# Performance work log

Measured on AMD Instinct MI355X. Metric: run time of the kernel, lower is better.

## Reference

```python
import jax, jax.numpy as jnp
import numpy as np

N_USERS = 100000
N_MOVIES = 100000
N_EDGES = 1000000
HIDDEN = 128


def setup_inputs() -> dict:
    key = jax.random.key(0)
    k1, k2, k3, k4, k5, k6, k7 = jax.random.split(key, 7)
    user_features = jax.random.normal(k1, (N_USERS, HIDDEN), dtype=jnp.float32)
    movie_features = jax.random.normal(k2, (N_MOVIES, HIDDEN), dtype=jnp.float32)
    src = jax.random.randint(k3, (N_EDGES,), 0, N_USERS, dtype=jnp.int64 if jax.config.jax_enable_x64 else jnp.int32)
    dst = jax.random.randint(k4, (N_EDGES,), 0, N_MOVIES, dtype=jnp.int64 if jax.config.jax_enable_x64 else jnp.int32)
    edge_index = jnp.stack([src, dst], axis=0)
    # Linear(2*HIDDEN, HIDDEN) params, torch-style init (kaiming uniform ~ U(-1/sqrt(fan_in), 1/sqrt(fan_in)))
    b1_bound = 1.0 / np.sqrt(2 * HIDDEN)
    W1 = jax.random.uniform(k5, (2 * HIDDEN, HIDDEN), minval=-b1_bound, maxval=b1_bound, dtype=jnp.float32)
    b1 = jax.random.uniform(k6, (HIDDEN,), minval=-b1_bound, maxval=b1_bound, dtype=jnp.float32)
    b2_bound = 1.0 / np.sqrt(HIDDEN)
    k8, k9 = jax.random.split(k7)
    W2 = jax.random.uniform(k8, (HIDDEN, 1), minval=-b2_bound, maxval=b2_bound, dtype=jnp.float32)
    b2 = jax.random.uniform(k9, (1,), minval=-b2_bound, maxval=b2_bound, dtype=jnp.float32)
    return {"user_features": user_features, "movie_features": movie_features,
            "edge_index": edge_index, "W1": W1, "b1": b1, "W2": W2, "b2": b2}


def reference(user_features, movie_features, edge_index, W1, b1, W2, b2):
    # Gather endpoint features per edge: [E, H] each
    u = user_features[edge_index[0]]
    m = movie_features[edge_index[1]]
    edge_feats = jnp.concatenate([u, m], axis=1)  # [E, 2H]
    h = jax.nn.relu(edge_feats @ W1 + b1)         # [E, H]
    out = h @ W2 + b2                             # [E, 1]
    return out.reshape(-1)
```

## Files before the change

### kernel.cpp

```cpp
#include <hip/hip_runtime.h>
#include <hip/hip_bf16.h>

typedef short s8v __attribute__((ext_vector_type(8)));
typedef float f4v __attribute__((ext_vector_type(4)));

__device__ __forceinline__ unsigned int bfround(float f) {
    unsigned int x = __float_as_uint(f);
    return (x + 0x7fffu + ((x >> 16) & 1u)) >> 16;
}

__device__ __forceinline__ float i8f(unsigned int w, int k) {
    return (float)((int)(signed char)(w >> (8 * k)));
}

__global__ __launch_bounds__(256) void pack_w(const float* __restrict__ W1,
                                              uint4* __restrict__ WF)
{
    const int half = blockIdx.x;
    #pragma unroll
    for (int iter = 0; iter < 8; ++iter) {
        int idx  = iter * 256 + threadIdx.x;
        int lane = idx & 63;
        int t    = (idx >> 6) & 7;
        int c    = idx >> 9;
        int q = lane >> 4, m = lane & 15;
        unsigned int w[4];
        #pragma unroll
        for (int jj = 0; jj < 4; ++jj) {
            float lo = W1[(size_t)(half * 128 + c * 32 + q * 8 + 2 * jj    ) * 128 + t * 16 + m];
            float hi = W1[(size_t)(half * 128 + c * 32 + q * 8 + 2 * jj + 1) * 128 + t * 16 + m];
            w[jj] = bfround(lo) | (bfround(hi) << 16);
        }
        WF[(size_t)half * 2048 + idx] = make_uint4(w[0], w[1], w[2], w[3]);
    }
}

__global__ __launch_bounds__(256, 3) void proj_kernel(
    const float* __restrict__ userf, const float* __restrict__ movief,
    const uint4* __restrict__ WF, const float* __restrict__ b1,
    uint2* __restrict__ Pu, uint2* __restrict__ Pm,
    float* __restrict__ SU, float* __restrict__ SM, int ntiles)
{
    const int half = blockIdx.x & 1;
    const int tile = (blockIdx.x >> 1) * 4 + (threadIdx.x >> 6);
    if (tile >= ntiles) return;
    const float* __restrict__ feat = half ? movief : userf;
    uint2* __restrict__ P = half ? Pm : Pu;
    float* __restrict__ S = half ? SM : SU;

    const int lane = threadIdx.x & 63;
    const int m    = lane & 15;
    const int q    = lane >> 4;

    const float4* arow = (const float4*)feat + (size_t)tile * 512;
    float4 a[4][2];
    #pragma unroll
    for (int c = 0; c < 4; ++c) {
        a[c][0] = arow[m * 32 + c * 8 + q * 2 + 0];
        a[c][1] = arow[m * 32 + c * 8 + q * 2 + 1];
    }

    float bias_v[8];
    #pragma unroll
    for (int t = 0; t < 8; ++t)
        bias_v[t] = half ? b1[t * 16 + m] : 0.0f;

    f4v acc[8];
    #pragma unroll
    for (int t = 0; t < 8; ++t)
        acc[t] = (f4v){bias_v[t], bias_v[t], bias_v[t], bias_v[t]};

    const uint4* wf = WF + (size_t)half * 2048;
    #pragma unroll
    for (int c = 0; c < 4; ++c) {
        uint4 fr[8];
        #pragma unroll
        for (int t = 0; t < 8; ++t)
            fr[t] = wf[(c * 8 + t) * 64 + lane];

        s8v af;
        af[0] = (short)bfround(a[c][0].x); af[1] = (short)bfround(a[c][0].y);
        af[2] = (short)bfround(a[c][0].z); af[3] = (short)bfround(a[c][0].w);
        af[4] = (short)bfround(a[c][1].x); af[5] = (short)bfround(a[c][1].y);
        af[6] = (short)bfround(a[c][1].z); af[7] = (short)bfround(a[c][1].w);

        #pragma unroll
        for (int t = 0; t < 8; ++t)
            acc[t] = __builtin_amdgcn_mfma_f32_16x16x32_bf16(af, *(const s8v*)&fr[t], acc[t], 0, 0, 0);
    }

    #pragma unroll
    for (int r = 0; r < 4; ++r) {
        float mx = 0.0f;
        #pragma unroll
        for (int t = 0; t < 8; ++t) mx = fmaxf(mx, fabsf(acc[t][r]));
        #pragma unroll
        for (int off = 1; off < 16; off <<= 1)
            mx = fmaxf(mx, __shfl_xor(mx, off, 64));
        float inv = mx > 0.0f ? 127.0f / mx : 0.0f;

        unsigned int lo = 0, hi = 0;
        #pragma unroll
        for (int t = 0; t < 4; ++t) {
            lo |= ((unsigned int)(__float2int_rn(acc[t][r]     * inv) & 0xff)) << (8 * t);
            hi |= ((unsigned int)(__float2int_rn(acc[t + 4][r] * inv) & 0xff)) << (8 * t);
        }
        int row = tile * 16 + q * 4 + r;
        P[(size_t)row * 16 + m] = make_uint2(lo, hi);
        if (m == 0) S[row] = mx * (1.0f / 127.0f);
    }
}

__global__ __launch_bounds__(256) void edge_kernel(
    const int* __restrict__ src, const int* __restrict__ dst,
    const uint2* __restrict__ Pu, const uint2* __restrict__ Pm,
    const float* __restrict__ SU, const float* __restrict__ SM,
    const float* __restrict__ W2, const float* __restrict__ b2,
    float* __restrict__ out)
{
    const int lane = threadIdx.x & 63;
    const int L    = lane & 15;
    const int g    = lane >> 4;
    const int eg   = (blockIdx.x * 4 + (threadIdx.x >> 6)) * 16 + g * 4;

    float w2v[8];
    #pragma unroll
    for (int j = 0; j < 8; ++j) w2v[j] = W2[j * 16 + L];

    int si[4], di[4];
    #pragma unroll
    for (int i = 0; i < 4; ++i) { si[i] = src[eg + i]; di[i] = dst[eg + i]; }

    uint2 pu[4], pm[4];
    float scu[4], scm[4];
    #pragma unroll
    for (int i = 0; i < 4; ++i) {
        pu[i] = Pu[(size_t)si[i] * 16 + L];
        pm[i] = Pm[(size_t)di[i] * 16 + L];
        scu[i] = SU[si[i]];
        scm[i] = SM[di[i]];
    }

    float res[4];
    #pragma unroll
    for (int i = 0; i < 4; ++i) {
        const unsigned int uw[2] = {pu[i].x, pu[i].y};
        const unsigned int mw[2] = {pm[i].x, pm[i].y};
        float acc = 0.0f;
        #pragma unroll
        for (int v = 0; v < 2; ++v) {
            #pragma unroll
            for (int k = 0; k < 4; ++k) {
                float h = fmaf(scu[i], i8f(uw[v], k), scm[i] * i8f(mw[v], k));
                acc = fmaf(fmaxf(h, 0.0f), w2v[v * 4 + k], acc);
            }
        }
        #pragma unroll
        for (int off = 1; off < 16; off <<= 1)
            acc += __shfl_xor(acc, off, 64);
        res[i] = acc;
    }

    if (L == 0) {
        float bb = b2[0];
        *(float4*)(out + eg) = make_float4(res[0] + bb, res[1] + bb, res[2] + bb, res[3] + bb);
    }
}

extern "C" void kernel_launch(void* const* d_in, const int* in_sizes, int n_in,
                              void* d_out, int out_size, void* d_ws, size_t ws_size,
                              hipStream_t stream) {
    const float* userf  = (const float*)d_in[0];
    const float* movief = (const float*)d_in[1];
    const int*   eidx   = (const int*)d_in[2];
    const float* W1     = (const float*)d_in[3];
    const float* b1     = (const float*)d_in[4];
    const float* W2     = (const float*)d_in[5];
    const float* b2     = (const float*)d_in[6];
    float* out = (float*)d_out;

    const int NU = in_sizes[0] / 128;
    const int NM = in_sizes[1] / 128;
    const int E  = in_sizes[2] / 2;

    uint2* Pu = (uint2*)d_ws;
    uint2* Pm = Pu + (size_t)NU * 16;
    float* SU = (float*)(Pm + (size_t)NM * 16);
    float* SM = SU + NU;
    uint4* WF = (uint4*)(SM + NM);

    const int ntiles = NU / 16;
    const int nblk   = 2 * ((ntiles + 3) / 4);

    pack_w<<<2, 256, 0, stream>>>(W1, WF);
    proj_kernel<<<nblk, 256, 0, stream>>>(userf, movief, WF, b1, Pu, Pm, SU, SM, ntiles);
    edge_kernel<<<E / 64, 256, 0, stream>>>(eidx, eidx + E, Pu, Pm, SU, SM, W2, b2, out);
}
```

Baseline: 192.9 us.

## Make projection kernel persistent with prefetch of next tile's features

The projection kernel now launches a fixed 1024 blocks, and each wave loops over tiles in a grid-stride pattern. While it computes the current tile, it loads the feature rows for the next one, so global-load latency overlaps with MFMA work. The per-element bf16 rounding is also replaced by the packed __float22bfloat162_rn conversion. The launch-bounds occupancy hint is dropped, and the prefetch buffer adds register pressure that could lower occupancy.

Result: no change. 192.3 us (-0.3%).

```diff
diff --git a/kernel.cpp b/kernel.cpp
--- a/kernel.cpp
+++ b/kernel.cpp
@@ -8,7 +8,10 @@
     unsigned int x = __float_as_uint(f);
     return (x + 0x7fffu + ((x >> 16) & 1u)) >> 16;
 }
-
+__device__ __forceinline__ unsigned int pkbf(float x, float y) {
+    __hip_bfloat162 h = __float22bfloat162_rn(make_float2(x, y));
+    return *(unsigned int*)&h;
+}
 __device__ __forceinline__ float i8f(unsigned int w, int k) {
     return (float)((int)(signed char)(w >> (8 * k)));
 }
@@ -35,80 +38,103 @@
     }
 }
 
-__global__ __launch_bounds__(256, 3) void proj_kernel(
+__global__ __launch_bounds__(256) void proj_kernel(
     const float* __restrict__ userf, const float* __restrict__ movief,
     const uint4* __restrict__ WF, const float* __restrict__ b1,
     uint2* __restrict__ Pu, uint2* __restrict__ Pm,
-    float* __restrict__ SU, float* __restrict__ SM, int ntiles)
+    float* __restrict__ SU, float* __restrict__ SM,
+    int ntiles, int bph)
 {
-    const int half = blockIdx.x & 1;
-    const int tile = (blockIdx.x >> 1) * 4 + (threadIdx.x >> 6);
-    if (tile >= ntiles) return;
+    const int half = blockIdx.x >= bph;
+    const int bid  = half ? blockIdx.x - bph : blockIdx.x;
     const float* __restrict__ feat = half ? movief : userf;
     uint2* __restrict__ P = half ? Pm : Pu;
     float* __restrict__ S = half ? SM : SU;
+    const uint4* __restrict__ wf = WF + (size_t)half * 2048;
 
     const int lane = threadIdx.x & 63;
     const int m    = lane & 15;
     const int q    = lane >> 4;
 
-    const float4* arow = (const float4*)feat + (size_t)tile * 512;
-    float4 a[4][2];
-    #pragma unroll
-    for (int c = 0; c < 4; ++c) {
-        a[c][0] = arow[m * 32 + c * 8 + q * 2 + 0];
-        a[c][1] = arow[m * 32 + c * 8 + q * 2 + 1];
-    }
-
     float bias_v[8];
     #pragma unroll
     for (int t = 0; t < 8; ++t)
         bias_v[t] = half ? b1[t * 16 + m] : 0.0f;
 
-    f4v acc[8];
-    #pragma unroll
-    for (int t = 0; t < 8; ++t)
-        acc[t] = (f4v){bias_v[t], bias_v[t], bias_v[t], bias_v[t]};
-
-    const uint4* wf = WF + (size_t)half * 2048;
-    #pragma unroll
-    for (int c = 0; c < 4; ++c) {
-        uint4 fr[8];
+    const int wid = bid * 4 + (threadIdx.x >> 6);
+    const int nw  = bph * 4;
+
+#define LOAD_A(dst, t_) do {                                          \
+        const float4* arow_ = (const float4*)feat + (size_t)(t_) * 512; \
+        _Pragma("unroll")                                             \
+        for (int c_ = 0; c_ < 4; ++c_) {                              \
+            dst[c_][0] = arow_[m * 32 + c_ * 8 + q * 2 + 0];          \
+            dst[c_][1] = arow_[m * 32 + c_ * 8 + q * 2 + 1];          \
+        }                                                             \
+    } while (0)
+
+    float4 a[4][2];
+    int tile = wid;
+    if (tile < ntiles) LOAD_A(a, tile);
+
+    while (tile < ntiles) {
+        const int nxt = tile + nw;
+        float4 an[4][2];
+        if (nxt < ntiles) LOAD_A(an, nxt);
+
+        f4v acc[8];
         #pragma unroll
         for (int t = 0; t < 8; ++t)
-            fr[t] = wf[(c * 8 + t) * 64 + lane];
-
-        s8v af;
-        af[0] = (short)bfround(a[c][0].x); af[1] = (short)bfround(a[c][0].y);
-        af[2] = (short)bfround(a[c][0].z); af[3] = (short)bfround(a[c][0].w);
-        af[4] = (short)bfround(a[c][1].x); af[5] = (short)bfround(a[c][1].y);
-        af[6] = (short)bfround(a[c][1].z); af[7] = (short)bfround(a[c][1].w);
-
-        #pragma unroll
-        for (int t = 0; t < 8; ++t)
-            acc[t] = __builtin_amdgcn_mfma_f32_16x16x32_bf16(af, *(const s8v*)&fr[t], acc[t], 0, 0, 0);
-    }
-
-    #pragma unroll
-    for (int r = 0; r < 4; ++r) {
-        float mx = 0.0f;
-        #pragma unroll
-        for (int t = 0; t < 8; ++t) mx = fmaxf(mx, fabsf(acc[t][r]));
-        #pragma unroll
-        for (int off = 1; off < 16; off <<= 1)
-            mx = fmaxf(mx, __shfl_xor(mx, off, 64));
-        float inv = mx > 0.0f ? 127.0f / mx : 0.0f;
-
-        unsigned int lo = 0, hi = 0;
-        #pragma unroll
-        for (int t = 0; t < 4; ++t) {
-            lo |= ((unsigned int)(__float2int_rn(acc[t][r]     * inv) & 0xff)) << (8 * t);
-            hi |= ((unsigned int)(__float2int_rn(acc[t + 4][r] * inv) & 0xff)) << (8 * t);
-        }
-        int row = tile * 16 + q * 4 + r;
-        P[(size_t)row * 16 + m] = make_uint2(lo, hi);
-        if (m == 0) S[row] = mx * (1.0f / 127.0f);
-    }
+            acc[t] = (f4v){bias_v[t], bias_v[t], bias_v[t], bias_v[t]};
+
+        #pragma unroll
+        for (int c = 0; c < 4; ++c) {
+            uint4 fr[8];
+            #pragma unroll
+            for (int t = 0; t < 8; ++t)
+                fr[t] = wf[(c * 8 + t) * 64 + lane];
+
+            uint4 aw;
+            aw.x = pkbf(a[c][0].x, a[c][0].y);
+            aw.y = pkbf(a[c][0].z, a[c][0].w);
+            aw.z = pkbf(a[c][1].x, a[c][1].y);
+            aw.w = pkbf(a[c][1].z, a[c][1].w);
+            s8v af = *(const s8v*)&aw;
+
+            #pragma unroll
+            for (int t = 0; t < 8; ++t)
+                acc[t] = __builtin_amdgcn_mfma_f32_16x16x32_bf16(af, *(const s8v*)&fr[t], acc[t], 0, 0, 0);
+        }
+
+        #pragma unroll
+        for (int r = 0; r < 4; ++r) {
+            float mx = 0.0f;
+            #pragma unroll
+            for (int t = 0; t < 8; ++t) mx = fmaxf(mx, fabsf(acc[t][r]));
+            #pragma unroll
+            for (int off = 1; off < 16; off <<= 1)
+                mx = fmaxf(mx, __shfl_xor(mx, off, 64));
+            float inv = mx > 0.0f ? 127.0f / mx : 0.0f;
+
+            unsigned int lo = 0, hi = 0;
+            #pragma unroll
+            for (int t = 0; t < 4; ++t) {
+                lo |= ((unsigned int)(__float2int_rn(acc[t][r]     * inv) & 0xff)) << (8 * t);
+                hi |= ((unsigned int)(__float2int_rn(acc[t + 4][r] * inv) & 0xff)) << (8 * t);
+            }
+            int row = tile * 16 + q * 4 + r;
+            P[(size_t)row * 16 + m] = make_uint2(lo, hi);
+            if (m == 0) S[row] = mx * (1.0f / 127.0f);
+        }
+
+        #pragma unroll
+        for (int c = 0; c < 4; ++c) {
+            a[c][0] = an[c][0];
+            a[c][1] = an[c][1];
+        }
+        tile = nxt;
+    }
+#undef LOAD_A
 }
 
 __global__ __launch_bounds__(256) void edge_kernel(
@@ -190,9 +216,9 @@
     uint4* WF = (uint4*)(SM + NM);
 
     const int ntiles = NU / 16;
-    const int nblk   = 2 * ((ntiles + 3) / 4);
+    const int bph    = 512;
 
     pack_w<<<2, 256, 0, stream>>>(W1, WF);
-    proj_kernel<<<nblk, 256, 0, stream>>>(userf, movief, WF, b1, Pu, Pm, SU, SM, ntiles);
+    proj_kernel<<<2 * bph, 256, 0, stream>>>(userf, movief, WF, b1, Pu, Pm, SU, SM, ntiles, bph);
     edge_kernel<<<E / 64, 256, 0, stream>>>(eidx, eidx + E, Pu, Pm, SU, SM, W2, b2, out);
 }
```

## Stage feature tiles through LDS with coalesced loads and packed bf16 conversion

Applied to the files above, without the earlier changes.

The projection kernel now loads each 16-row feature tile with fully coalesced float4 reads, converts pairs to bf16 with the packed intrinsic, and stores them to a padded LDS buffer. Each wave then reads its MFMA A-fragment from LDS, replacing the earlier strided per-lane global reads. Block-to-half mapping changes from interleaved to contiguous ranges, and the occupancy hint in launch bounds is dropped. The cost is 18KB of LDS per block plus extra LDS traffic, and there is no barrier because each wave only touches its own slice.

Result: no change. 189.9 us (-1.5%).

```diff
diff --git a/kernel.cpp b/kernel.cpp
--- a/kernel.cpp
+++ b/kernel.cpp
@@ -8,7 +8,10 @@
     unsigned int x = __float_as_uint(f);
     return (x + 0x7fffu + ((x >> 16) & 1u)) >> 16;
 }
-
+__device__ __forceinline__ unsigned int pkbf(float x, float y) {
+    __hip_bfloat162 h = __float22bfloat162_rn(make_float2(x, y));
+    return *(unsigned int*)&h;
+}
 __device__ __forceinline__ float i8f(unsigned int w, int k) {
     return (float)((int)(signed char)(w >> (8 * k)));
 }
@@ -35,54 +38,56 @@
     }
 }
 
-__global__ __launch_bounds__(256, 3) void proj_kernel(
+__global__ __launch_bounds__(256) void proj_kernel(
     const float* __restrict__ userf, const float* __restrict__ movief,
     const uint4* __restrict__ WF, const float* __restrict__ b1,
     uint2* __restrict__ Pu, uint2* __restrict__ Pm,
-    float* __restrict__ SU, float* __restrict__ SM, int ntiles)
+    float* __restrict__ SU, float* __restrict__ SM,
+    int ntiles, int bph)
 {
-    const int half = blockIdx.x & 1;
-    const int tile = (blockIdx.x >> 1) * 4 + (threadIdx.x >> 6);
+    __shared__ __align__(16) unsigned int lds[4608];
+
+    const int w    = threadIdx.x >> 6;
+    const int lane = threadIdx.x & 63;
+    const int half = blockIdx.x >= bph;
+    const int bid  = half ? blockIdx.x - bph : blockIdx.x;
+    const int tile = bid * 4 + w;
     if (tile >= ntiles) return;
+
     const float* __restrict__ feat = half ? movief : userf;
     uint2* __restrict__ P = half ? Pm : Pu;
     float* __restrict__ S = half ? SM : SU;
-
-    const int lane = threadIdx.x & 63;
-    const int m    = lane & 15;
-    const int q    = lane >> 4;
-
-    const float4* arow = (const float4*)feat + (size_t)tile * 512;
-    float4 a[4][2];
-    #pragma unroll
-    for (int c = 0; c < 4; ++c) {
-        a[c][0] = arow[m * 32 + c * 8 + q * 2 + 0];
-        a[c][1] = arow[m * 32 + c * 8 + q * 2 + 1];
-    }
-
-    float bias_v[8];
-    #pragma unroll
-    for (int t = 0; t < 8; ++t)
-        bias_v[t] = half ? b1[t * 16 + m] : 0.0f;
+    const uint4* __restrict__ wfh = WF + (size_t)half * 2048;
+
+    unsigned int* wl = lds + w * 1152;
+
+    const float4* tbase = (const float4*)feat + (size_t)tile * 512;
+    #pragma unroll
+    for (int p = 0; p < 8; ++p) {
+        float4 v = tbase[p * 64 + lane];
+        int r  = (p * 64 + lane) >> 5;
+        int cc = lane & 31;
+        *(uint2*)&wl[r * 72 + cc * 2] = make_uint2(pkbf(v.x, v.y), pkbf(v.z, v.w));
+    }
+
+    const int m = lane & 15;
+    const int q = lane >> 4;
 
     f4v acc[8];
     #pragma unroll
-    for (int t = 0; t < 8; ++t)
-        acc[t] = (f4v){bias_v[t], bias_v[t], bias_v[t], bias_v[t]};
-
-    const uint4* wf = WF + (size_t)half * 2048;
+    for (int t = 0; t < 8; ++t) {
+        float bv = half ? b1[t * 16 + m] : 0.0f;
+        acc[t] = (f4v){bv, bv, bv, bv};
+    }
+
     #pragma unroll
     for (int c = 0; c < 4; ++c) {
         uint4 fr[8];
         #pragma unroll
         for (int t = 0; t < 8; ++t)
-            fr[t] = wf[(c * 8 + t) * 64 + lane];
-
-        s8v af;
-        af[0] = (short)bfround(a[c][0].x); af[1] = (short)bfround(a[c][0].y);
-        af[2] = (short)bfround(a[c][0].z); af[3] = (short)bfround(a[c][0].w);
-        af[4] = (short)bfround(a[c][1].x); af[5] = (short)bfround(a[c][1].y);
-        af[6] = (short)bfround(a[c][1].z); af[7] = (short)bfround(a[c][1].w);
+            fr[t] = wfh[(c * 8 + t) * 64 + lane];
+
+        s8v af = *(const s8v*)&wl[m * 72 + c * 16 + q * 4];
 
         #pragma unroll
         for (int t = 0; t < 8; ++t)
@@ -190,9 +195,9 @@
     uint4* WF = (uint4*)(SM + NM);
 
     const int ntiles = NU / 16;
-    const int nblk   = 2 * ((ntiles + 3) / 4);
+    const int bph    = (ntiles + 3) / 4;
 
     pack_w<<<2, 256, 0, stream>>>(W1, WF);
-    proj_kernel<<<nblk, 256, 0, stream>>>(userf, movief, WF, b1, Pu, Pm, SU, SM, ntiles);
+    proj_kernel<<<2 * bph, 256, 0, stream>>>(userf, movief, WF, b1, Pu, Pm, SU, SM, ntiles, bph);
     edge_kernel<<<E / 64, 256, 0, stream>>>(eidx, eidx + E, Pu, Pm, SU, SM, W2, b2, out);
 }
```
